# Kernel tuning notes

Measured on AMD Instinct MI355X. Metric: run time of the kernel, lower is better.

## Reference

```python
import jax, jax.numpy as jnp
import numpy as np

DIM = 1024
N_HIDDEN = 64
NUM_HEADS = 16
B, S = 4, 1024
# original torch code: scale = sqrt(n_hidden // num_heads) = sqrt(64 // 16) = 2.0
SCALE = float(np.sqrt(N_HIDDEN // NUM_HEADS))


def setup_inputs() -> dict:
    key = jax.random.key(0)
    ks = jax.random.split(key, 10)
    lim = 1.0 / np.sqrt(DIM)          # nn.Linear default init range
    lim_o = 1.0 / np.sqrt(N_HIDDEN * NUM_HEADS)
    u = lambda k, shape, l: jax.random.uniform(k, shape, jnp.float32, -l, l)
    x = jax.random.normal(ks[0], (B, S, DIM), jnp.float32)
    attn_mask = jax.random.randint(ks[1], (B, S, S), 0, 2).astype(jnp.int32)
    # stacked per-head projection weights: [H, dim, n_hidden]
    Wq = u(ks[2], (NUM_HEADS, DIM, N_HIDDEN), lim)
    bq = u(ks[3], (NUM_HEADS, N_HIDDEN), lim)
    Wk = u(ks[4], (NUM_HEADS, DIM, N_HIDDEN), lim)
    bk = u(ks[5], (NUM_HEADS, N_HIDDEN), lim)
    Wv = u(ks[6], (NUM_HEADS, DIM, N_HIDDEN), lim)
    bv = u(ks[7], (NUM_HEADS, N_HIDDEN), lim)
    Wo = u(ks[8], (NUM_HEADS * N_HIDDEN, DIM), lim_o)
    bo = u(ks[9], (DIM,), lim_o)
    return {"x": x, "attn_mask": attn_mask, "Wq": Wq, "bq": bq,
            "Wk": Wk, "bk": bk, "Wv": Wv, "bv": bv, "Wo": Wo, "bo": bo}


def reference(x, attn_mask, Wq, bq, Wk, bk, Wv, bv, Wo, bo):
    # batched QKV across all heads (replaces the per-head Python loop)
    Q = jnp.einsum('bsd,hde->bhse', x, Wq) + bq[None, :, None, :]
    K = jnp.einsum('bsd,hde->bhse', x, Wk) + bk[None, :, None, :]
    V = jnp.einsum('bsd,hde->bhse', x, Wv) + bv[None, :, None, :]
    scores = jnp.einsum('bhse,bhte->bhst', Q, K) / SCALE
    alpha = jax.nn.softmax(scores, axis=-1)
    # faithful to original: zero out masked entries AFTER softmax, no renorm
    alpha = jnp.where(attn_mask[:, None, :, :] == 0, 0.0, alpha)  # [B,H,S,S]
    out = jnp.einsum('bhst,bhte->bhse', alpha, V)                 # [B,H,S,E]
    # torch.cat over heads on last dim == reshape to [B,S,H*E] in head order
    concat = out.transpose(0, 2, 1, 3).reshape(B, S, NUM_HEADS * N_HIDDEN)
    attn_output = concat @ Wo + bo                                # [B,S,dim]
    return attn_output, alpha
```

## Files before the change

kernel.cpp:

```cpp
#include <hip/hip_runtime.h>
#include <stdint.h>

#define S_LEN 1024
#define DIM   1024
#define NHID  64
#define NHEAD 16
#define NB    4

typedef __bf16 bf16x8 __attribute__((ext_vector_type(8)));
typedef float  f32x4  __attribute__((ext_vector_type(4)));
typedef unsigned short u16;

__device__ __forceinline__ u16 f2b(float f) {
  unsigned u = __float_as_uint(f);
  u += 0x7FFFu + ((u >> 16) & 1u);
  return (u16)(u >> 16);
}

__device__ __forceinline__ f32x4 mfma16(bf16x8 a, bf16x8 b, f32x4 c) {
  return __builtin_amdgcn_mfma_f32_16x16x32_bf16(a, b, c, 0, 0, 0);
}

__device__ __forceinline__ void transpose_tile(const float* __restrict__ ip,
                                               u16* __restrict__ op,
                                               int R, int C, int r0, int c0,
                                               float (*tile)[65], int t) {
  {
    int col = t & 63, rr = t >> 6;
#pragma unroll
    for (int p = 0; p < 8; ++p) {
      int r = p * 4 + rr;
      tile[r][col] = ip[(size_t)(r0 + r) * C + c0 + col];
    }
  }
  __syncthreads();
  {
    int d = t & 31, er = t >> 5;
#pragma unroll
    for (int p = 0; p < 8; ++p) {
      int e = p * 8 + er;
      op[(size_t)(c0 + e) * R + r0 + d] = f2b(tile[d][e]);
    }
  }
}

__global__ __launch_bounds__(256) void k_prep(const float* __restrict__ x,
                                              const int* __restrict__ mask,
                                              const float* __restrict__ Wq,
                                              const float* __restrict__ Wk,
                                              const float* __restrict__ Wv,
                                              const float* __restrict__ Wo,
                                              u16* __restrict__ xb,
                                              uint32_t* __restrict__ mbits,
                                              u16* __restrict__ Wtb,
                                              u16* __restrict__ Wotb) {
  __shared__ float tile[32][65];
  int blk = blockIdx.x, t = threadIdx.x;
  if (blk < 4096) {
    int i = blk * 256 + t;
    float4 v = ((const float4*)x)[i];
    ushort4 o;
    o.x = f2b(v.x); o.y = f2b(v.y); o.z = f2b(v.z); o.w = f2b(v.w);
    ((ushort4*)xb)[i] = o;
  } else if (blk < 4608) {
    int w = (blk - 4096) * 256 + t;
    const int4* mp = (const int4*)mask + (size_t)w * 8;
    uint32_t v = 0;
#pragma unroll
    for (int i = 0; i < 8; ++i) {
      int4 m = mp[i];
      v |= (m.x != 0 ? 1u : 0u) << (i * 4 + 0);
      v |= (m.y != 0 ? 1u : 0u) << (i * 4 + 1);
      v |= (m.z != 0 ? 1u : 0u) << (i * 4 + 2);
      v |= (m.w != 0 ? 1u : 0u) << (i * 4 + 3);
    }
    mbits[w] = v;
  } else if (blk < 6144) {
    int rel = blk - 4608;
    int sel = rel >> 9;
    int r2 = rel & 511;
    int batch = r2 >> 5;
    int r0 = (r2 & 31) * 32;
    const float* W = (sel == 0) ? Wq : (sel == 1) ? Wk : Wv;
    transpose_tile(W + (size_t)batch * 65536,
                   Wtb + (size_t)sel * 1048576 + (size_t)batch * 65536,
                   1024, 64, r0, 0, tile, t);
  } else {
    int rel = blk - 6144;
    int r0 = (rel >> 4) * 32;
    int c0 = (rel & 15) * 64;
    transpose_tile(Wo, Wotb, 1024, 1024, r0, c0, tile, t);
  }
}

__global__ __launch_bounds__(256) void k_qkv(const u16* __restrict__ xb,
                                             const u16* __restrict__ Wtb,
                                             const float* __restrict__ bq,
                                             const float* __restrict__ bk,
                                             const float* __restrict__ bv,
                                             u16* __restrict__ Qb,
                                             u16* __restrict__ Kb,
                                             u16* __restrict__ Vtb) {
  __shared__ __align__(16) char lds[32768];
  int t = threadIdx.x, w = t >> 6, lane = t & 63;
  int l15 = lane & 15, l4 = lane >> 4;
  int m0 = blockIdx.x * 128, n0 = blockIdx.y * 128, sel = blockIdx.z;
  const u16* Wh = Wtb + (size_t)sel * (NHEAD * NHID * DIM);
  int wr = w >> 1, wc = w & 1;

  f32x4 acc[4][4];
  const f32x4 fz = {0.f, 0.f, 0.f, 0.f};
#pragma unroll
  for (int i = 0; i < 4; ++i)
#pragma unroll
    for (int j = 0; j < 4; ++j) acc[i][j] = fz;

  for (int kk = 0; kk < 16; ++kk) {
    int k0 = kk * 64;
#pragma unroll
    for (int c = 0; c < 4; ++c) {
      int idx = c * 256 + t, r = idx >> 3, cb = idx & 7;
      int4 v = *(const int4*)(xb + (size_t)(m0 + r) * DIM + k0 + cb * 8);
      *(int4*)(lds + r * 128 + ((cb * 16) ^ ((r & 7) << 4))) = v;
    }
#pragma unroll
    for (int c = 0; c < 4; ++c) {
      int idx = c * 256 + t, r = idx >> 3, cb = idx & 7;
      int4 v = *(const int4*)(Wh + (size_t)(n0 + r) * DIM + k0 + cb * 8);
      *(int4*)(lds + 16384 + r * 128 + ((cb * 16) ^ ((r & 7) << 4))) = v;
    }
    __syncthreads();
    bf16x8 a[4][2], bb[4][2];
#pragma unroll
    for (int mf = 0; mf < 4; ++mf)
#pragma unroll
      for (int kc = 0; kc < 2; ++kc) {
        int row = wr * 64 + mf * 16 + l15;
        int kb = kc * 64 + l4 * 16;
        a[mf][kc] = *(const bf16x8*)(lds + row * 128 + (kb ^ ((row & 7) << 4)));
      }
#pragma unroll
    for (int nf = 0; nf < 4; ++nf)
#pragma unroll
      for (int kc = 0; kc < 2; ++kc) {
        int row = wc * 64 + nf * 16 + l15;
        int kb = kc * 64 + l4 * 16;
        bb[nf][kc] = *(const bf16x8*)(lds + 16384 + row * 128 + (kb ^ ((row & 7) << 4)));
      }
#pragma unroll
    for (int kc = 0; kc < 2; ++kc)
#pragma unroll
      for (int mf = 0; mf < 4; ++mf)
#pragma unroll
        for (int nf = 0; nf < 4; ++nf)
          acc[mf][nf] = mfma16(a[mf][kc], bb[nf][kc], acc[mf][nf]);
    __syncthreads();
  }

  const float* bias = (sel == 0) ? bq : (sel == 1) ? bk : bv;
  float postScale = (sel == 0) ? 0.5f : 1.0f;
#pragma unroll
  for (int nf = 0; nf < 4; ++nf) {
    int n = n0 + wc * 64 + nf * 16 + l15;
    int h = n >> 6, e = n & 63;
    float bv_ = bias[n];
#pragma unroll
    for (int mf = 0; mf < 4; ++mf) {
      int mrow0 = m0 + wr * 64 + mf * 16 + l4 * 4;
      int b_ = mrow0 >> 10, s0 = mrow0 & 1023;
      if (sel == 2) {
        ushort4 pk;
        pk.x = f2b(acc[mf][nf][0] + bv_);
        pk.y = f2b(acc[mf][nf][1] + bv_);
        pk.z = f2b(acc[mf][nf][2] + bv_);
        pk.w = f2b(acc[mf][nf][3] + bv_);
        *(ushort4*)(Vtb + ((size_t)(b_ * NHEAD + h) * NHID + e) * S_LEN + s0) = pk;
      } else {
        u16* dst = (sel == 0) ? Qb : Kb;
#pragma unroll
        for (int j = 0; j < 4; ++j)
          dst[((size_t)(b_ * NHEAD + h) * S_LEN + s0 + j) * NHID + e] =
              f2b((acc[mf][nf][j] + bv_) * postScale);
      }
    }
  }
}

__global__ __launch_bounds__(256) void k_attn(const u16* __restrict__ Qb,
                                              const u16* __restrict__ Kb,
                                              const u16* __restrict__ Vtb,
                                              const uint32_t* __restrict__ mbitsG,
                                              float* __restrict__ alphaOut,
                                              u16* __restrict__ Ob) {
  __shared__ __align__(16) char smem[33024];
  float* redS = (float*)(smem + 32768);
  int t = threadIdx.x, w = t >> 6, lane = t & 63;
  int l15 = lane & 15, l4 = lane >> 4;
  int q0 = blockIdx.x * 16;
  int bh = blockIdx.y, b = bh >> 4, hh = bh & 15;
  const u16* Qh = Qb + (size_t)bh * S_LEN * NHID;
  const u16* Kh = Kb + (size_t)bh * S_LEN * NHID;
  const u16* Vh = Vtb + (size_t)bh * NHID * S_LEN;
  int kbase = w * 256;

  const uint32_t* mrow = mbitsG + ((size_t)b * S_LEN + q0 + l15) * 32 + w * 8;
  uint4 mw0 = *(const uint4*)(mrow);
  uint4 mw1 = *(const uint4*)(mrow + 4);

  bf16x8 aq[2];
#pragma unroll
  for (int ec = 0; ec < 2; ++ec)
    aq[ec] = *(const bf16x8*)(Qh + (size_t)(q0 + l15) * NHID + ec * 32 + l4 * 8);

  const f32x4 fz = {0.f, 0.f, 0.f, 0.f};

  float s0 = 0.f, s1 = 0.f, s2 = 0.f, s3 = 0.f;
#pragma unroll
  for (int kf = 0; kf < 16; ++kf) {
    int key = kbase + kf * 16 + l15;
    bf16x8 kb0 = *(const bf16x8*)(Kh + (size_t)key * NHID + l4 * 8);
    bf16x8 kb1 = *(const bf16x8*)(Kh + (size_t)key * NHID + 32 + l4 * 8);
    f32x4 sct = fz;
    sct = mfma16(kb0, aq[0], sct);
    sct = mfma16(kb1, aq[1], sct);
    float e0 = __expf(sct[0]);
    float e1 = __expf(sct[1]);
    float e2 = __expf(sct[2]);
    float e3 = __expf(sct[3]);
    s0 += e0; s1 += e1; s2 += e2; s3 += e3;
    uint32_t mword;
    switch (kf >> 1) {
      case 0: mword = mw0.x; break;
      case 1: mword = mw0.y; break;
      case 2: mword = mw0.z; break;
      case 3: mword = mw0.w; break;
      case 4: mword = mw1.x; break;
      case 5: mword = mw1.y; break;
      case 6: mword = mw1.z; break;
      default: mword = mw1.w; break;
    }
    int bbase = ((kf & 1) << 4) + l4 * 4;
    uint32_t am01 = (((mword >> (bbase + 0)) & 1u) ? 0x0000FFFFu : 0u) |
                    (((mword >> (bbase + 1)) & 1u) ? 0xFFFF0000u : 0u);
    uint32_t am23 = (((mword >> (bbase + 2)) & 1u) ? 0x0000FFFFu : 0u) |
                    (((mword >> (bbase + 3)) & 1u) ? 0xFFFF0000u : 0u);
    uint2 pk;
    pk.x = ((uint32_t)f2b(e0) | ((uint32_t)f2b(e1) << 16)) & am01;
    pk.y = ((uint32_t)f2b(e2) | ((uint32_t)f2b(e3) << 16)) & am23;
    *(uint2*)(smem + l15 * 2048 +
              (((kbase + kf * 16 + l4 * 4) * 2) ^ ((l15 & 7) << 4))) = pk;
  }
  float ls = (s0 + s1) + (s2 + s3);
  ls += __shfl_xor(ls, 16);
  ls += __shfl_xor(ls, 32);
  if (lane < 16) redS[w * 16 + l15] = ls;
  __syncthreads();

  float* abW = alphaOut + (size_t)bh * S_LEN * S_LEN;
  f32x4 o[4];
#pragma unroll
  for (int ef = 0; ef < 4; ++ef) o[ef] = fz;

  auto rw = [&](int rr) {
    int r = w * 4 + rr;
    float invr = 1.f / (redS[r] + redS[16 + r] + redS[32 + r] + redS[48 + r]);
    float* dst = abW + (size_t)(q0 + r) * S_LEN;
#pragma unroll
    for (int seg = 0; seg < 4; ++seg) {
      int raw = seg * 512 + lane * 8;
      int boff = raw ^ ((r & 7) << 4);
      uint2 pk = *(const uint2*)(smem + r * 2048 + boff);
      f32x4 av;
      av[0] = __uint_as_float(pk.x << 16) * invr;
      av[1] = __uint_as_float(pk.x & 0xFFFF0000u) * invr;
      av[2] = __uint_as_float(pk.y << 16) * invr;
      av[3] = __uint_as_float(pk.y & 0xFFFF0000u) * invr;
      __builtin_nontemporal_store(av, (f32x4*)(dst + (raw >> 1)));
    }
  };
  auto pvc = [&](int c) {
#pragma unroll
    for (int kc2 = 0; kc2 < 2; ++kc2) {
      bf16x8 pa = *(const bf16x8*)(smem + l15 * 2048 +
          ((((kbase + c * 64 + kc2 * 32) * 2) + l4 * 16) ^ ((l15 & 7) << 4)));
#pragma unroll
      for (int ef = 0; ef < 4; ++ef) {
        int e = ef * 16 + l15;
        bf16x8 vb = *(const bf16x8*)(Vh + (size_t)e * S_LEN + kbase + c * 64 +
                                     kc2 * 32 + l4 * 8);
        o[ef] = mfma16(pa, vb, o[ef]);
      }
    }
  };

  rw(0); pvc(0);
  rw(1); pvc(1);
  rw(2); pvc(2);
  rw(3); pvc(3);

  __syncthreads();
  float* redO = (float*)smem;
#pragma unroll
  for (int ef = 0; ef < 4; ++ef)
#pragma unroll
    for (int j = 0; j < 4; ++j)
      redO[w * 1024 + (l4 * 4 + j) * 64 + ef * 16 + l15] = o[ef][j];
  __syncthreads();
  {
    int e = t & 63, r4 = t >> 6;
#pragma unroll
    for (int p = 0; p < 4; ++p) {
      int r = p * 4 + r4;
      float invr = 1.f / (redS[r] + redS[16 + r] + redS[32 + r] + redS[48 + r]);
      float s4 = redO[r * 64 + e] + redO[1024 + r * 64 + e] +
                 redO[2048 + r * 64 + e] + redO[3072 + r * 64 + e];
      Ob[(size_t)(b * S_LEN + q0 + r) * DIM + hh * NHID + e] = f2b(s4 * invr);
    }
  }
}

__global__ __launch_bounds__(256) void k_oproj(const u16* __restrict__ Ob,
                                               const u16* __restrict__ Wotb,
                                               const float* __restrict__ bo,
                                               float* __restrict__ out) {
  __shared__ __align__(16) char lds[32768];
  int t = threadIdx.x, w = t >> 6, lane = t & 63;
  int l15 = lane & 15, l4 = lane >> 4;
  int m0 = blockIdx.x * 128, n0 = blockIdx.y * 128;
  int wr = w >> 1, wc = w & 1;
  f32x4 acc[4][4];
  const f32x4 fz = {0.f, 0.f, 0.f, 0.f};
#pragma unroll
  for (int i = 0; i < 4; ++i)
#pragma unroll
    for (int j = 0; j < 4; ++j) acc[i][j] = fz;

  for (int kk = 0; kk < 16; ++kk) {
    int k0 = kk * 64;
#pragma unroll
    for (int c = 0; c < 4; ++c) {
      int idx = c * 256 + t, r = idx >> 3, cb = idx & 7;
      int4 v = *(const int4*)(Ob + (size_t)(m0 + r) * DIM + k0 + cb * 8);
      *(int4*)(lds + r * 128 + ((cb * 16) ^ ((r & 7) << 4))) = v;
    }
#pragma unroll
    for (int c = 0; c < 4; ++c) {
      int idx = c * 256 + t, r = idx >> 3, cb = idx & 7;
      int4 v = *(const int4*)(Wotb + (size_t)(n0 + r) * DIM + k0 + cb * 8);
      *(int4*)(lds + 16384 + r * 128 + ((cb * 16) ^ ((r & 7) << 4))) = v;
    }
    __syncthreads();
    bf16x8 a[4][2], bb[4][2];
#pragma unroll
    for (int mf = 0; mf < 4; ++mf)
#pragma unroll
      for (int kc = 0; kc < 2; ++kc) {
        int row = wr * 64 + mf * 16 + l15;
        int kb = kc * 64 + l4 * 16;
        a[mf][kc] = *(const bf16x8*)(lds + row * 128 + (kb ^ ((row & 7) << 4)));
      }
#pragma unroll
    for (int nf = 0; nf < 4; ++nf)
#pragma unroll
      for (int kc = 0; kc < 2; ++kc) {
        int row = wc * 64 + nf * 16 + l15;
        int kb = kc * 64 + l4 * 16;
        bb[nf][kc] = *(const bf16x8*)(lds + 16384 + row * 128 + (kb ^ ((row & 7) << 4)));
      }
#pragma unroll
    for (int kc = 0; kc < 2; ++kc)
#pragma unroll
      for (int mf = 0; mf < 4; ++mf)
#pragma unroll
        for (int nf = 0; nf < 4; ++nf)
          acc[mf][nf] = mfma16(a[mf][kc], bb[nf][kc], acc[mf][nf]);
    __syncthreads();
  }
#pragma unroll
  for (int nf = 0; nf < 4; ++nf) {
    int n = n0 + wc * 64 + nf * 16 + l15;
    float bv_ = bo[n];
#pragma unroll
    for (int mf = 0; mf < 4; ++mf)
#pragma unroll
      for (int j = 0; j < 4; ++j) {
        int m = m0 + wr * 64 + mf * 16 + l4 * 4 + j;
        out[(size_t)m * DIM + n] = acc[mf][nf][j] + bv_;
      }
  }
}

extern "C" void kernel_launch(void* const* d_in, const int* in_sizes, int n_in,
                              void* d_out, int out_size, void* d_ws, size_t ws_size,
                              hipStream_t stream) {
  const float* x    = (const float*)d_in[0];
  const int*   mask = (const int*)d_in[1];
  const float* Wq   = (const float*)d_in[2];
  const float* bq   = (const float*)d_in[3];
  const float* Wk   = (const float*)d_in[4];
  const float* bk   = (const float*)d_in[5];
  const float* Wv   = (const float*)d_in[6];
  const float* bv   = (const float*)d_in[7];
  const float* Wo   = (const float*)d_in[8];
  const float* bo   = (const float*)d_in[9];
  float* out = (float*)d_out;
  float* alphaOut = out + (size_t)NB * S_LEN * DIM;

  char* ws = (char*)d_ws;
  u16* xb    = (u16*)(ws);
  u16* Wtb   = (u16*)(ws + 8388608);
  u16* Wotb  = (u16*)(ws + 14680064);
  u16* Qb    = (u16*)(ws + 16777216);
  u16* Kb    = (u16*)(ws + 25165824);
  u16* Vtb   = (u16*)(ws + 33554432);
  u16* Ob    = (u16*)(ws + 41943040);
  uint32_t* mbits = (uint32_t*)(ws + 50331648);

  k_prep<<<6656, 256, 0, stream>>>(x, mask, Wq, Wk, Wv, Wo, xb, mbits, Wtb, Wotb);
  k_qkv<<<dim3(32, 8, 3), 256, 0, stream>>>(xb, Wtb, bq, bk, bv, Qb, Kb, Vtb);
  k_attn<<<dim3(64, 64), 256, 0, stream>>>(Qb, Kb, Vtb, mbits, alphaOut, Ob);
  k_oproj<<<dim3(32, 8), 256, 0, stream>>>(Ob, Wotb, bo, out);
}
```

Measured before the change: 213.0 us.

## Halve attention query tile to 8 rows, cutting LDS and doubling blocks

```diff
diff --git a/kernel.cpp b/kernel.cpp
--- a/kernel.cpp
+++ b/kernel.cpp
@@ -192,29 +192,29 @@
                                               const uint32_t* __restrict__ mbitsG,
                                               float* __restrict__ alphaOut,
                                               u16* __restrict__ Ob) {
-  __shared__ __align__(16) char smem[33024];
-  float* redS = (float*)(smem + 32768);
+  __shared__ __align__(16) char smem[16384];
   int t = threadIdx.x, w = t >> 6, lane = t & 63;
   int l15 = lane & 15, l4 = lane >> 4;
-  int q0 = blockIdx.x * 16;
+  int q0 = blockIdx.x * 8;
   int bh = blockIdx.y, b = bh >> 4, hh = bh & 15;
   const u16* Qh = Qb + (size_t)bh * S_LEN * NHID;
   const u16* Kh = Kb + (size_t)bh * S_LEN * NHID;
   const u16* Vh = Vtb + (size_t)bh * NHID * S_LEN;
   int kbase = w * 256;
-
-  const uint32_t* mrow = mbitsG + ((size_t)b * S_LEN + q0 + l15) * 32 + w * 8;
+  int myrow = l15 & 7;
+
+  const uint32_t* mrow = mbitsG + ((size_t)b * S_LEN + q0 + myrow) * 32 + w * 8;
   uint4 mw0 = *(const uint4*)(mrow);
   uint4 mw1 = *(const uint4*)(mrow + 4);
 
+  int qq = q0 + l15; if (qq > 1023) qq = 1023;
   bf16x8 aq[2];
 #pragma unroll
   for (int ec = 0; ec < 2; ++ec)
-    aq[ec] = *(const bf16x8*)(Qh + (size_t)(q0 + l15) * NHID + ec * 32 + l4 * 8);
+    aq[ec] = *(const bf16x8*)(Qh + (size_t)qq * NHID + ec * 32 + l4 * 8);
 
   const f32x4 fz = {0.f, 0.f, 0.f, 0.f};
 
-  float s0 = 0.f, s1 = 0.f, s2 = 0.f, s3 = 0.f;
 #pragma unroll
   for (int kf = 0; kf < 16; ++kf) {
     int key = kbase + kf * 16 + l15;
@@ -223,66 +223,85 @@
     f32x4 sct = fz;
     sct = mfma16(kb0, aq[0], sct);
     sct = mfma16(kb1, aq[1], sct);
-    float e0 = __expf(sct[0]);
-    float e1 = __expf(sct[1]);
-    float e2 = __expf(sct[2]);
-    float e3 = __expf(sct[3]);
-    s0 += e0; s1 += e1; s2 += e2; s3 += e3;
-    uint32_t mword;
-    switch (kf >> 1) {
-      case 0: mword = mw0.x; break;
-      case 1: mword = mw0.y; break;
-      case 2: mword = mw0.z; break;
-      case 3: mword = mw0.w; break;
-      case 4: mword = mw1.x; break;
-      case 5: mword = mw1.y; break;
-      case 6: mword = mw1.z; break;
-      default: mword = mw1.w; break;
-    }
-    int bbase = ((kf & 1) << 4) + l4 * 4;
-    uint32_t am01 = (((mword >> (bbase + 0)) & 1u) ? 0x0000FFFFu : 0u) |
-                    (((mword >> (bbase + 1)) & 1u) ? 0xFFFF0000u : 0u);
-    uint32_t am23 = (((mword >> (bbase + 2)) & 1u) ? 0x0000FFFFu : 0u) |
-                    (((mword >> (bbase + 3)) & 1u) ? 0xFFFF0000u : 0u);
     uint2 pk;
-    pk.x = ((uint32_t)f2b(e0) | ((uint32_t)f2b(e1) << 16)) & am01;
-    pk.y = ((uint32_t)f2b(e2) | ((uint32_t)f2b(e3) << 16)) & am23;
-    *(uint2*)(smem + l15 * 2048 +
-              (((kbase + kf * 16 + l4 * 4) * 2) ^ ((l15 & 7) << 4))) = pk;
-  }
-  float ls = (s0 + s1) + (s2 + s3);
-  ls += __shfl_xor(ls, 16);
-  ls += __shfl_xor(ls, 32);
-  if (lane < 16) redS[w * 16 + l15] = ls;
+    pk.x = (uint32_t)f2b(__expf(sct[0])) | ((uint32_t)f2b(__expf(sct[1])) << 16);
+    pk.y = (uint32_t)f2b(__expf(sct[2])) | ((uint32_t)f2b(__expf(sct[3])) << 16);
+    if (l15 < 8)
+      *(uint2*)(smem + l15 * 2048 +
+                (((kbase + kf * 16 + l4 * 4) * 2) ^ (l15 << 4))) = pk;
+  }
   __syncthreads();
 
   float* abW = alphaOut + (size_t)bh * S_LEN * S_LEN;
-  f32x4 o[4];
-#pragma unroll
-  for (int ef = 0; ef < 4; ++ef) o[ef] = fz;
-
-  auto rw = [&](int rr) {
-    int r = w * 4 + rr;
-    float invr = 1.f / (redS[r] + redS[16 + r] + redS[32 + r] + redS[48 + r]);
+  float invv[2];
+
+#pragma unroll
+  for (int rr = 0; rr < 2; ++rr) {
+    int r = w * 2 + rr;
+    float ps = 0.f;
+#pragma unroll
+    for (int i = 0; i < 4; ++i) {
+      int raw = i * 512 + lane * 8;
+      uint2 pk = *(const uint2*)(smem + r * 2048 + (raw ^ (r << 4)));
+      ps += __uint_as_float(pk.x << 16) + __uint_as_float(pk.x & 0xFFFF0000u) +
+            __uint_as_float(pk.y << 16) + __uint_as_float(pk.y & 0xFFFF0000u);
+    }
+#pragma unroll
+    for (int msk = 1; msk < 64; msk <<= 1) ps += __shfl_xor(ps, msk);
+    float inv = 1.f / ps;
+    invv[rr] = inv;
     float* dst = abW + (size_t)(q0 + r) * S_LEN;
+    const uint32_t* mrowR = mbitsG + ((size_t)b * S_LEN + q0 + r) * 32;
 #pragma unroll
     for (int seg = 0; seg < 4; ++seg) {
       int raw = seg * 512 + lane * 8;
-      int boff = raw ^ ((r & 7) << 4);
-      uint2 pk = *(const uint2*)(smem + r * 2048 + boff);
+      uint2 pk = *(const uint2*)(smem + r * 2048 + (raw ^ (r << 4)));
+      uint32_t mword = mrowR[seg * 8 + (lane >> 3)];
+      int bbase = (lane & 7) * 4;
+      uint32_t am01 = (((mword >> (bbase + 0)) & 1u) ? 0x0000FFFFu : 0u) |
+                      (((mword >> (bbase + 1)) & 1u) ? 0xFFFF0000u : 0u);
+      uint32_t am23 = (((mword >> (bbase + 2)) & 1u) ? 0x0000FFFFu : 0u) |
+                      (((mword >> (bbase + 3)) & 1u) ? 0xFFFF0000u : 0u);
+      uint32_t mp01 = pk.x & am01, mp23 = pk.y & am23;
       f32x4 av;
-      av[0] = __uint_as_float(pk.x << 16) * invr;
-      av[1] = __uint_as_float(pk.x & 0xFFFF0000u) * invr;
-      av[2] = __uint_as_float(pk.y << 16) * invr;
-      av[3] = __uint_as_float(pk.y & 0xFFFF0000u) * invr;
+      av[0] = __uint_as_float(mp01 << 16) * inv;
+      av[1] = __uint_as_float(mp01 & 0xFFFF0000u) * inv;
+      av[2] = __uint_as_float(mp23 << 16) * inv;
+      av[3] = __uint_as_float(mp23 & 0xFFFF0000u) * inv;
       __builtin_nontemporal_store(av, (f32x4*)(dst + (raw >> 1)));
     }
-  };
-  auto pvc = [&](int c) {
+  }
+
+  f32x4 o[4];
+#pragma unroll
+  for (int ef = 0; ef < 4; ++ef) o[ef] = fz;
+#pragma unroll
+  for (int c = 0; c < 4; ++c) {
 #pragma unroll
     for (int kc2 = 0; kc2 < 2; ++kc2) {
-      bf16x8 pa = *(const bf16x8*)(smem + l15 * 2048 +
-          ((((kbase + c * 64 + kc2 * 32) * 2) + l4 * 16) ^ ((l15 & 7) << 4)));
+      int kb_ = kbase + c * 64 + kc2 * 32 + l4 * 8;
+      bf16x8 pa = *(const bf16x8*)(smem + myrow * 2048 +
+                                   (((kb_) * 2) ^ (myrow << 4)));
+      uint32_t mword;
+      switch (c * 2 + kc2) {
+        case 0: mword = mw0.x; break;
+        case 1: mword = mw0.y; break;
+        case 2: mword = mw0.z; break;
+        case 3: mword = mw0.w; break;
+        case 4: mword = mw1.x; break;
+        case 5: mword = mw1.y; break;
+        case 6: mword = mw1.z; break;
+        default: mword = mw1.w; break;
+      }
+      uint32_t bits = (mword >> (l4 * 8)) & 0xFFu;
+      uint32_t pm[4];
+#pragma unroll
+      for (int i = 0; i < 4; ++i)
+        pm[i] = (((bits >> (2 * i)) & 1u) ? 0x0000FFFFu : 0u) |
+                (((bits >> (2 * i + 1)) & 1u) ? 0xFFFF0000u : 0u);
+      uint32_t* pw = (uint32_t*)&pa;
+#pragma unroll
+      for (int i = 0; i < 4; ++i) pw[i] &= pm[i];
 #pragma unroll
       for (int ef = 0; ef < 4; ++ef) {
         int e = ef * 16 + l15;
@@ -291,30 +310,29 @@
         o[ef] = mfma16(pa, vb, o[ef]);
       }
     }
-  };
-
-  rw(0); pvc(0);
-  rw(1); pvc(1);
-  rw(2); pvc(2);
-  rw(3); pvc(3);
+  }
 
   __syncthreads();
   float* redO = (float*)smem;
-#pragma unroll
-  for (int ef = 0; ef < 4; ++ef)
-#pragma unroll
-    for (int j = 0; j < 4; ++j)
-      redO[w * 1024 + (l4 * 4 + j) * 64 + ef * 16 + l15] = o[ef][j];
+  float* invL = (float*)(smem + 8192);
+  if (lane == 0) { invL[w * 2] = invv[0]; invL[w * 2 + 1] = invv[1]; }
+  if (l4 < 2) {
+#pragma unroll
+    for (int ef = 0; ef < 4; ++ef)
+#pragma unroll
+      for (int j = 0; j < 4; ++j)
+        redO[w * 512 + (l4 * 4 + j) * 64 + ef * 16 + l15] = o[ef][j];
+  }
   __syncthreads();
   {
-    int e = t & 63, r4 = t >> 6;
-#pragma unroll
-    for (int p = 0; p < 4; ++p) {
-      int r = p * 4 + r4;
-      float invr = 1.f / (redS[r] + redS[16 + r] + redS[32 + r] + redS[48 + r]);
-      float s4 = redO[r * 64 + e] + redO[1024 + r * 64 + e] +
-                 redO[2048 + r * 64 + e] + redO[3072 + r * 64 + e];
-      Ob[(size_t)(b * S_LEN + q0 + r) * DIM + hh * NHID + e] = f2b(s4 * invr);
+    int e = t & 63, r2 = t >> 6;
+#pragma unroll
+    for (int p = 0; p < 2; ++p) {
+      int r = p * 4 + r2;
+      float s4 = redO[r * 64 + e] + redO[512 + r * 64 + e] +
+                 redO[1024 + r * 64 + e] + redO[1536 + r * 64 + e];
+      Ob[(size_t)(b * S_LEN + q0 + r) * DIM + hh * NHID + e] =
+          f2b(s4 * invL[r]);
     }
   }
 }
@@ -418,6 +436,6 @@
 
   k_prep<<<6656, 256, 0, stream>>>(x, mask, Wq, Wk, Wv, Wo, xb, mbits, Wtb, Wotb);
   k_qkv<<<dim3(32, 8, 3), 256, 0, stream>>>(xb, Wtb, bq, bk, bv, Qb, Kb, Vtb);
-  k_attn<<<dim3(64, 64), 256, 0, stream>>>(Qb, Kb, Vtb, mbits, alphaOut, Ob);
+  k_attn<<<dim3(128, 64), 256, 0, stream>>>(Qb, Kb, Vtb, mbits, alphaOut, Ob);
   k_oproj<<<dim3(32, 8), 256, 0, stream>>>(Ob, Wotb, bo, out);
 }
```

Result: slower. 332.3 us, median of 2 (+56.0%).
